# Performance work log

Hardware: AMD Instinct MI355X
Metric: run time of the kernel (lower is better)

## Reference

```python
import jax, jax.numpy as jnp
import numpy as np
from functools import partial

# --- constants from module init / yolov5 NMS conventions ---
CONF_THRES = 0.25
IOU_THRES = 0.45
PATCH_CONF = 0.001
GN = jnp.array([640.0, 640.0, 640.0, 640.0])  # img_size[[1,0,1,0]]
MAX_WH = 4096.0       # per-class NMS offset trick
K_CLEAN = 256         # fixed-size cap for clean detections (max_det=1000 effectively)
K_PATCH = 1024        # fixed-size cap for patch detections (max_det=30000 effectively)
MAXDET_CLEAN = 1000
MAXDET_PATCH = 30000
B, N, NC = 8, 25200, 80


def xywh2xyxy(x):
    xy, wh = x[..., :2], x[..., 2:4]
    return jnp.concatenate([xy - wh * 0.5, xy + wh * 0.5], axis=-1)


def pairwise_iou(a, b):
    # a: [A,4], b: [B,4] -> [A,B] jaccard overlap (same math as IoU.get_iou)
    tl = jnp.maximum(a[:, None, :2], b[None, :, :2])
    br = jnp.minimum(a[:, None, 2:], b[None, :, 2:])
    wh = jnp.clip(br - tl, 0.0)
    inter = wh[..., 0] * wh[..., 1]
    area_a = (a[:, 2] - a[:, 0]) * (a[:, 3] - a[:, 1])
    area_b = (b[:, 2] - b[:, 0]) * (b[:, 3] - b[:, 1])
    return inter / (area_a[:, None] + area_b[None, :] - inter)


def greedy_nms(iou_mat, valid, iou_thres):
    # iou_mat: [K,K] (score-sorted order), valid: [K] bool. Greedy suppression.
    K = valid.shape[0]
    j = jnp.arange(K)

    def body(i, keep):
        suppress = keep[i] & (iou_mat[i] > iou_thres) & (j > i)
        return keep & ~suppress

    return jax.lax.fori_loop(0, K, body, valid)


def _nms_single(pred, conf_thres, K, max_det):
    # pred: [N, 5+nc] raw yolov5 prediction for one image
    boxes = xywh2xyxy(pred[:, :4])
    obj = pred[:, 4]
    cls_scores = pred[:, 5:] * obj[:, None]          # conf = obj * cls
    conf = cls_scores.max(axis=-1)
    cls = jnp.argmax(cls_scores, axis=-1).astype(pred.dtype)
    valid = (obj > conf_thres) & (conf > conf_thres)
    mscore = jnp.where(valid, conf, -1.0)
    _, idx = jax.lax.top_k(mscore, K)                # fixed-size candidate prefilter
    bk, ck, vk = boxes[idx], cls[idx], valid[idx]
    off_boxes = bk + (ck * MAX_WH)[:, None]          # class-offset NMS
    iou = pairwise_iou(off_boxes, off_boxes)
    keep = greedy_nms(jax.lax.stop_gradient(iou), vk, IOU_THRES)
    keep = keep & (jnp.cumsum(keep.astype(jnp.int32)) <= max_det)
    return bk, ck, keep


def _forward(output_clean, output_patch):
    nms_clean = jax.vmap(lambda p: _nms_single(p, CONF_THRES, K_CLEAN, MAXDET_CLEAN))
    nms_patch = jax.vmap(lambda p: _nms_single(p, PATCH_CONF, K_PATCH, MAXDET_PATCH))
    bc, cc, kc = nms_clean(output_clean)   # [B,Kc,4],[B,Kc],[B,Kc]
    bp, cp, kp = nms_patch(output_patch)   # [B,Kp,4],[B,Kp],[B,Kp]
    bc_n = bc / GN
    bp_n = bp / GN

    def per_img(bp_i, cp_i, kp_i, bc_i, cc_i, kc_i):
        iou = pairwise_iou(bp_i, bc_i)                       # [Kp, Kc]
        match = kp_i[:, None] & (cp_i[:, None] == cc_i[None, :])
        tm = jnp.max(jnp.where(match, iou, 0.0), axis=0)     # max IoU per clean det
        return jnp.sum(jnp.where(kc_i, tm, 0.0)), jnp.sum(kc_i.astype(jnp.float32))

    sums, counts = jax.vmap(per_img)(bp_n, cp, kp, bc_n, cc, kc)
    total, cnt = sums.sum(), counts.sum()
    return jnp.where(cnt > 0, 1.0 - total / jnp.maximum(cnt, 1.0), 1.0)


def setup_inputs() -> dict:
    key = jax.random.key(0)
    k1, k2 = jax.random.split(key)

    def make(k):
        kxy, kwh, ko, kc = jax.random.split(k, 4)
        xy = jax.random.uniform(kxy, (B, N, 2)) * 608.0 + 16.0   # centers in-frame
        wh = jax.random.uniform(kwh, (B, N, 2)) * 96.0 + 8.0     # plausible box sizes
        obj = jax.random.uniform(ko, (B, N, 1))
        cls = jax.random.uniform(kc, (B, N, NC))
        return jnp.concatenate([xy, wh, obj, cls], axis=-1)

    return {"output_clean": make(k1), "output_patch": make(k2)}


def reference(output_clean, output_patch):
    return _forward(output_clean, output_patch)
```

## Files before the change

kernel.cpp:

```cpp
#include <hip/hip_runtime.h>

#define N_ANCH 25200
#define NCLS   80
#define ROW    85
#define NIMG   16
#define KMAX   1024
#define NBINS  4096
#define CAND_CAP 4096
#define SC2_RPC 16
#define SC2_CPI 1575
#define SC2_CHUNKS (NIMG * SC2_CPI)
#define SC2_CFLOATS (SC2_RPC * ROW)
#define SC2_BLOCKS 1792
#define PCHUNK 64
#define CCNT_STRIDE 16

typedef unsigned long long u64;
typedef unsigned int u32;

#define OFF_KEYS 0ull
#define OFF_HIST 3225600ull
#define OFF_TBIN 3487744ull
#define OFF_CCNT 3487808ull
#define OFF_SUMS 3488832ull
#define OFF_CNTS 3488864ull
#define OFF_CAND 3488896ull
#define OFF_SEL  4013184ull
#define OFF_BOX  4144256ull
#define OFF_CLS  4406400ull
#define OFF_RINIT 4471936ull
#define OFF_KEEP 4473984ull
#define WS_NEED  4539520ull
#define ZERO_BYTES (262144ull + 64 + 1024 + 32 + 32)

#define DMA16(gsrc, ldst) \
    __builtin_amdgcn_global_load_lds( \
        (const __attribute__((address_space(1))) void*)(gsrc), \
        (__attribute__((address_space(3))) void*)(ldst), 16, 0, 0)

__device__ __forceinline__ int key_bin(u64 key) {
    u32 hi = (u32)(key >> 32);
    if (hi == 0u) return 0;
    float conf = __uint_as_float(hi - 0x40000000u);
    int b = 1 + (int)(conf * 4093.0f);
    return b > 4094 ? 4094 : b;
}

__device__ __forceinline__ u64 readlane64(u64 v, int src) {
    u32 lo = (u32)__builtin_amdgcn_readlane((int)(u32)(v & 0xffffffffull), src);
    u32 hi = (u32)__builtin_amdgcn_readlane((int)(u32)(v >> 32), src);
    return ((u64)hi << 32) | (u64)lo;
}

__device__ __forceinline__ u64 shfl64_xor(u64 v, int m) {
    int lo = __shfl_xor((int)(u32)(v & 0xffffffffull), m, 64);
    int hi = __shfl_xor((int)(u32)(v >> 32), m, 64);
    return ((u64)(u32)hi << 32) | (u64)(u32)lo;
}

__device__ __forceinline__ void sc_issue(const float* __restrict__ clean,
                                         const float* __restrict__ patch,
                                         int c, int lane, float* buf)
{
    const int b = c / SC2_CPI;
    const int ch = c - b * SC2_CPI;
    const float* g = ((b < 8) ? clean + (size_t)b * N_ANCH * ROW
                              : patch + (size_t)(b - 8) * N_ANCH * ROW)
                     + (size_t)ch * SC2_CFLOATS;
    #pragma unroll
    for (int u = 0; u < 5; ++u)
        DMA16(g + u * 256 + lane * 4, buf + u * 256);
    if (lane < 20)
        DMA16(g + 5 * 256 + lane * 4, buf + 5 * 256);
}

__device__ __forceinline__ void sc_compute(int c, int lane,
                                           const float* buf, u64* __restrict__ keys)
{
    const int b = c / SC2_CPI;
    const int ch = c - b * SC2_CPI;
    const int r = lane & 15, h = lane >> 4;
    const float* p = buf + r * ROW;
    const float obj = p[4];
    float best = -1.0f; int bc = 0;
    #pragma unroll
    for (int d = 0; d < 20; ++d) {
        const float s = p[5 + h * 20 + d] * obj;
        if (s > best) { best = s; bc = h * 20 + d; }
    }
    #pragma unroll
    for (int m = 16; m <= 32; m <<= 1) {
        const float o = __shfl_xor(best, m, 64);
        const int  oc = __shfl_xor(bc, m, 64);
        if (o > best || (o == best && oc < bc)) { best = o; bc = oc; }
    }
    if (h == 0) {
        const int n = ch * SC2_RPC + r;
        const float th = (b < 8) ? 0.25f : 0.001f;
        const bool valid = (obj > th) && (best > th);
        const u32 hi = valid ? (__float_as_uint(best) + 0x40000000u) : 0u;
        const u32 nbar = 32767u - (u32)n;
        keys[(size_t)b * N_ANCH + n] =
            ((u64)hi << 32) | ((u64)nbar << 8) | (u64)(u32)bc;
    }
}

__global__ __launch_bounds__(128) void k_score(const float* __restrict__ clean,
                                               const float* __restrict__ patch,
                                               u64* __restrict__ keys)
{
    __shared__ float lds[2][2][SC2_CFLOATS];
    const int wv = threadIdx.x >> 6, lane = threadIdx.x & 63;
    const int wid = blockIdx.x * 2 + wv;
    const int stride = SC2_BLOCKS * 2;
    int cur = 0;
    sc_issue(clean, patch, wid, lane, &lds[wv][0][0]);
    for (int c = wid; c < SC2_CHUNKS; c += stride) {
        const int cn = c + stride;
        if (cn < SC2_CHUNKS) {
            sc_issue(clean, patch, cn, lane, &lds[wv][cur ^ 1][0]);
            asm volatile("s_waitcnt vmcnt(6)" ::: "memory");
        } else {
            asm volatile("s_waitcnt vmcnt(0)" ::: "memory");
        }
        __builtin_amdgcn_sched_barrier(0);
        sc_compute(c, lane, &lds[wv][cur][0], keys);
        cur ^= 1;
    }
}

__global__ __launch_bounds__(256) void k_hist(const u64* __restrict__ keys,
                                              int* __restrict__ hist)
{
    __shared__ int h[NBINS];
    const int b = blockIdx.x;
    for (int i = threadIdx.x; i < NBINS; i += 256) h[i] = 0;
    __syncthreads();
    const int start = blockIdx.y * 1575;
    const u64* kp = keys + (size_t)b * N_ANCH;
    for (int i = start + threadIdx.x; i < start + 1575; i += 256)
        atomicAdd(&h[key_bin(kp[i])], 1);
    __syncthreads();
    for (int i = threadIdx.x; i < NBINS; i += 256)
        if (h[i]) atomicAdd(&hist[b * NBINS + i], h[i]);
}

__global__ __launch_bounds__(1024) void k_thresh(const int* __restrict__ hist,
                                                 int* __restrict__ tbin)
{
    __shared__ int arr[1024];
    const int b = blockIdx.x;
    const int t = threadIdx.x;
    int hh[4];
    hh[0] = hist[b * NBINS + 4 * t + 0];
    hh[1] = hist[b * NBINS + 4 * t + 1];
    hh[2] = hist[b * NBINS + 4 * t + 2];
    hh[3] = hist[b * NBINS + 4 * t + 3];
    const int r = hh[0] + hh[1] + hh[2] + hh[3];
    arr[t] = r;
    __syncthreads();
    for (int off = 1; off < 1024; off <<= 1) {
        int v = (t + off < 1024) ? arr[t + off] : 0;
        __syncthreads();
        arr[t] += v;
        __syncthreads();
    }
    const int K = (b < 8) ? 256 : 1024;
    int cb = arr[t] - r;
    for (int d = 3; d >= 0; --d) {
        int ca = cb + hh[d];
        if (cb < K && ca >= K) tbin[b] = 4 * t + d;
        cb = ca;
    }
}

__global__ __launch_bounds__(256) void k_compact(const u64* __restrict__ keys,
                                                 const int* __restrict__ tbin,
                                                 int* __restrict__ ccnt,
                                                 u64* __restrict__ cand)
{
    const int b = blockIdx.x;
    const int T = tbin[b];
    const u64* kp = keys + (size_t)b * N_ANCH;
    const int start = blockIdx.y * 1575;
    const int lane = threadIdx.x & 63;
    #pragma unroll
    for (int it = 0; it < 7; ++it) {
        const int off = it * 256 + threadIdx.x;
        const bool in = off < 1575;
        const u64 key = in ? kp[start + off] : 0ull;
        const bool cnd = in && (key_bin(key) >= T);
        const u64 bal = __ballot(cnd);
        if (bal) {
            int base = 0;
            if (lane == 0) base = atomicAdd(&ccnt[b * CCNT_STRIDE], __popcll(bal));
            base = __shfl(base, 0, 64);
            if (cnd) {
                const int pos = base + __popcll(bal & ((1ull << lane) - 1ull));
                if (pos < CAND_CAP) cand[(size_t)b * CAND_CAP + pos] = key;
            }
        }
    }
}

__global__ __launch_bounds__(1024) void k_sort(const u64* __restrict__ cand,
                                               const int* __restrict__ ccnt,
                                               u64* __restrict__ sel)
{
    __shared__ u64 sk[CAND_CAP];
    const int b = blockIdx.x;
    const int C = min(ccnt[b * CCNT_STRIDE], CAND_CAP);
    const int t = threadIdx.x;
    u64 e0, e1, e2, e3;
    e0 = (t < C) ? cand[(size_t)b * CAND_CAP + t] : 0ull;
    e1 = (1024 + t < C) ? cand[(size_t)b * CAND_CAP + 1024 + t] : 0ull;
    e2 = (2048 + t < C) ? cand[(size_t)b * CAND_CAP + 2048 + t] : 0ull;
    e3 = (3072 + t < C) ? cand[(size_t)b * CAND_CAP + 3072 + t] : 0ull;

    #define CSWAP_D(a, c) { if ((a) < (c)) { u64 _t = (a); (a) = (c); (c) = _t; } }
    #define CSWAP_A(a, c) { if ((a) > (c)) { u64 _t = (a); (a) = (c); (c) = _t; } }

    for (int k = 2; k <= 4096; k <<= 1) {
        for (int j = k >> 1; j > 0; j >>= 1) {
            if (j >= 1024) {
                if (j == 2048) {
                    CSWAP_D(e0, e2); CSWAP_D(e1, e3);
                } else {
                    if (k == 4096) { CSWAP_D(e0, e1); CSWAP_D(e2, e3); }
                    else           { CSWAP_D(e0, e1); CSWAP_A(e2, e3); }
                }
            } else if (j >= 64) {
                __syncthreads();
                sk[t] = e0; sk[1024 + t] = e1; sk[2048 + t] = e2; sk[3072 + t] = e3;
                __syncthreads();
                const int tp = t ^ j;
                #pragma unroll
                for (int p = 0; p < 4; ++p) {
                    const int i = p * 1024 + t;
                    const u64 cv = (p == 0) ? e0 : (p == 1) ? e1 : (p == 2) ? e2 : e3;
                    const u64 o = sk[p * 1024 + tp];
                    const bool take_max = (((i & k) == 0) == ((t & j) == 0));
                    const u64 mx = cv > o ? cv : o;
                    const u64 mn = cv > o ? o : cv;
                    const u64 nv = take_max ? mx : mn;
                    if (p == 0) e0 = nv; else if (p == 1) e1 = nv;
                    else if (p == 2) e2 = nv; else e3 = nv;
                }
            } else {
                #pragma unroll
                for (int p = 0; p < 4; ++p) {
                    const int i = p * 1024 + t;
                    const u64 cv = (p == 0) ? e0 : (p == 1) ? e1 : (p == 2) ? e2 : e3;
                    const u64 o = shfl64_xor(cv, j);
                    const bool take_max = (((i & k) == 0) == ((t & j) == 0));
                    const u64 mx = cv > o ? cv : o;
                    const u64 mn = cv > o ? o : cv;
                    const u64 nv = take_max ? mx : mn;
                    if (p == 0) e0 = nv; else if (p == 1) e1 = nv;
                    else if (p == 2) e2 = nv; else e3 = nv;
                }
            }
        }
    }
    const int K = (b < 8) ? 256 : 1024;
    if (t < K) sel[b * KMAX + t] = e0;
    #undef CSWAP_D
    #undef CSWAP_A
}

__global__ __launch_bounds__(1024) void k_gather(const float* __restrict__ clean,
                                                 const float* __restrict__ patch,
                                                 const u64* __restrict__ sel,
                                                 float4* __restrict__ boxes,
                                                 int* __restrict__ cls,
                                                 u64* __restrict__ rinit)
{
    const int b = blockIdx.x;
    const int t = threadIdx.x;
    const int K = (b < 8) ? 256 : 1024;
    const u64 key = (t < K) ? sel[b * KMAX + t] : 0ull;
    const u32 hi = (u32)(key >> 32);
    const bool valid = (t < K) && (hi != 0u);
    u64 bal = __ballot(valid);
    if ((t & 63) == 0) rinit[b * 16 + (t >> 6)] = ~bal;
    if (t >= K) return;
    const int n = 32767 - (int)((key >> 8) & 0x7FFFu);
    const int c = (int)(key & 0x7Fu);
    const float* src = ((b < 8) ? (clean + (size_t)b * N_ANCH * ROW)
                                : (patch + (size_t)(b - 8) * N_ANCH * ROW)) + (size_t)n * ROW;
    const float x = src[0], y = src[1], w = src[2], h = src[3];
    boxes[b * KMAX + t] = make_float4(x - w * 0.5f, y - h * 0.5f, x + w * 0.5f, y + h * 0.5f);
    cls[b * KMAX + t] = c;
}

__global__ __launch_bounds__(1024) void k_nms_mask(const float4* __restrict__ boxes,
                                                   const int* __restrict__ cls,
                                                   u64* __restrict__ mask,
                                                   u64* __restrict__ diag)
{
    __shared__ float4 bx[KMAX];
    __shared__ float ar[KMAX];
    const int b = blockIdx.x;
    const int K = (b < 8) ? 256 : 1024;
    const int row0 = blockIdx.y * 64;
    if (row0 >= K) return;
    const int t = threadIdx.x;
    for (int i = t; i < K; i += 1024) {
        float4 v = boxes[b * KMAX + i];
        float off = (float)cls[b * KMAX + i] * 4096.0f;
        v.x += off; v.y += off; v.z += off; v.w += off;
        bx[i] = v;
        ar[i] = (v.z - v.x) * (v.w - v.y);
    }
    __syncthreads();
    const int w   = t >> 6;
    const int row = row0 + (t & 63);
    u64* dst = mask + ((size_t)b * KMAX + row) * 16 + w;
    if (((w << 6) + 63) <= row0 && row0 > 0) { *dst = 0ull; return; }
    const float4 bi = bx[row];
    const float ai = ar[row];
    const int jbase = w << 6;
    u64 m = 0;
    #pragma unroll 8
    for (int k = 0; k < 64; ++k) {
        const int j = jbase + k;
        const float4 bj = bx[j];
        const float ax = fmaxf(bi.x, bj.x), ay = fmaxf(bi.y, bj.y);
        const float bx2 = fminf(bi.z, bj.z), by2 = fminf(bi.w, bj.w);
        const float iw = fmaxf(bx2 - ax, 0.f), ih = fmaxf(by2 - ay, 0.f);
        const float inter = iw * ih;
        const float iou = inter / (ai + ar[j] - inter);
        if (j > row && iou > 0.45f) m |= (1ull << k);
    }
    *dst = m;
    if (w == (row0 >> 6)) diag[(size_t)b * KMAX + row] = m;
}

__global__ __launch_bounds__(1024) void k_nms_scan(const u64* __restrict__ mask,
                                                   const u64* __restrict__ diag,
                                                   const u64* __restrict__ rinit,
                                                   int* __restrict__ keep)
{
    extern __shared__ u64 smem[];
    const int b = blockIdx.x;
    const int K = (b < 8) ? 256 : 1024;
    const int W = K >> 6;
    const int t = threadIdx.x;
    u64* smask = smem;
    u64* sdiag = smem + (size_t)K * 16;
    {
        const float4* s4 = (const float4*)(mask + (size_t)b * KMAX * 16);
        float4* d4 = (float4*)smask;
        const int n4 = (K * 16) >> 1;
        for (int i = t; i < n4; i += 1024) d4[i] = s4[i];
        const float4* s4d = (const float4*)(diag + (size_t)b * KMAX);
        float4* d4d = (float4*)sdiag;
        for (int i = t; i < (K >> 1); i += 1024) d4d[i] = s4d[i];
    }
    __syncthreads();
    if (t >= 64) return;
    const int lane = t;
    const int q = lane >> 4;
    const int wl = lane & 15;
    u64 w_remv = rinit[b * 16 + wl];
    u64 ow = readlane64(w_remv, 0);
    u64 dj = sdiag[lane];
    for (int g = 0; g < W; ++g) {
        u64 nz = __ballot(dj != 0ull);
        u64 o = ow;
        while (nz) {
            const int j = (int)__builtin_ctzll(nz);
            nz &= nz - 1;
            if (!((o >> j) & 1ull)) o |= readlane64(dj, j);
        }
        const u64 kept = ~o;
        if (g + 1 < W) dj = sdiag[(g + 1) * 64 + lane];
        const u64* mrow = smask + (size_t)(g * 64 + q * 16) * 16 + wl;
        const u32 kg = (u32)((kept >> (q * 16)) & 0xFFFFull);
        u64 a0 = 0, a1 = 0;
        #pragma unroll
        for (int i = 0; i < 16; i += 2) {
            const u64 m0 = mrow[(size_t)(i + 0) * 16];
            const u64 m1 = mrow[(size_t)(i + 1) * 16];
            a0 |= ((kg >> i) & 1u) ? m0 : 0ull;
            a1 |= ((kg >> (i + 1)) & 1u) ? m1 : 0ull;
        }
        u64 part = a0 | a1;
        part |= shfl64_xor(part, 16);
        part |= shfl64_xor(part, 32);
        w_remv |= part;
        if (g + 1 < W) ow = readlane64(w_remv, g + 1);
    }
    if (lane < W) {
        #pragma unroll
        for (int k = 0; k < 64; ++k)
            keep[b * KMAX + lane * 64 + k] = (int)(((w_remv >> k) & 1) ^ 1ull);
    }
}

__global__ __launch_bounds__(256) void k_match_partial(const float4* __restrict__ boxes,
                                                       const int* __restrict__ cls,
                                                       const int* __restrict__ keep,
                                                       float* __restrict__ pmax)
{
    __shared__ float4 pb[PCHUNK];
    __shared__ float par[PCHUNK];
    __shared__ int pcls[PCHUNK];
    const int c = blockIdx.x;
    const int p = blockIdx.y;
    const int bp = 8 + c;
    const int t = threadIdx.x;
    if (t < PCHUNK) {
        const int i = p * PCHUNK + t;
        const float4 v = boxes[bp * KMAX + i];
        pb[t] = v;
        par[t] = (v.z - v.x) * (v.w - v.y);
        pcls[t] = keep[bp * KMAX + i] ? cls[bp * KMAX + i] : -1;
    }
    __syncthreads();
    const float4 bc = boxes[c * KMAX + t];
    const int cc = cls[c * KMAX + t];
    const float area_c = (bc.z - bc.x) * (bc.w - bc.y);
    float tm = 0.f;
    #pragma unroll 8
    for (int i = 0; i < PCHUNK; ++i) {
        const float4 bi = pb[i];
        const float ax = fmaxf(bi.x, bc.x), ay = fmaxf(bi.y, bc.y);
        const float bx2 = fminf(bi.z, bc.z), by2 = fminf(bi.w, bc.w);
        const float iw = fmaxf(bx2 - ax, 0.f), ih = fmaxf(by2 - ay, 0.f);
        const float inter = iw * ih;
        const float iou = inter / (par[i] + area_c - inter);
        tm = fmaxf(tm, (pcls[i] == cc) ? iou : 0.f);
    }
    pmax[(c * 16 + p) * 256 + t] = tm;
}

__global__ __launch_bounds__(256) void k_match_reduce(const float* __restrict__ pmax,
                                                      const int* __restrict__ keep,
                                                      float* __restrict__ sums,
                                                      float* __restrict__ cnts)
{
    __shared__ float red[8];
    const int c = blockIdx.x;
    const int t = threadIdx.x;
    float tm = 0.f;
    #pragma unroll
    for (int p = 0; p < 16; ++p)
        tm = fmaxf(tm, pmax[(c * 16 + p) * 256 + t]);
    const int kc = keep[c * KMAX + t];
    float val = kc ? tm : 0.f;
    float cv  = kc ? 1.f : 0.f;
    for (int off = 32; off > 0; off >>= 1) {
        val += __shfl_down(val, off);
        cv  += __shfl_down(cv, off);
    }
    const int wv = t >> 6, lane = t & 63;
    if (lane == 0) { red[wv] = val; red[4 + wv] = cv; }
    __syncthreads();
    if (t == 0) {
        sums[c] = red[0] + red[1] + red[2] + red[3];
        cnts[c] = red[4] + red[5] + red[6] + red[7];
    }
}

__global__ void k_final(const float* __restrict__ sums,
                        const float* __restrict__ cnts,
                        float* __restrict__ out)
{
    if (threadIdx.x == 0 && blockIdx.x == 0) {
        float total = 0.f, cnt = 0.f;
        for (int c = 0; c < 8; ++c) { total += sums[c]; cnt += cnts[c]; }
        out[0] = (cnt > 0.f) ? (1.0f - total / fmaxf(cnt, 1.0f)) : 1.0f;
    }
}

extern "C" void kernel_launch(void* const* d_in, const int* in_sizes, int n_in,
                              void* d_out, int out_size, void* d_ws, size_t ws_size,
                              hipStream_t stream)
{
    if (ws_size < WS_NEED) return;
    const float* clean = (const float*)d_in[0];
    const float* patch = (const float*)d_in[1];
    float* out = (float*)d_out;
    char* ws = (char*)d_ws;

    u64*    keys = (u64*)(ws + OFF_KEYS);
    u64*    mask = (u64*)(ws + OFF_KEYS);
    int*    hist = (int*)(ws + OFF_HIST);
    u64*    diag = (u64*)(ws + OFF_HIST);
    int*    tbin = (int*)(ws + OFF_TBIN);
    int*    ccnt = (int*)(ws + OFF_CCNT);
    float*  sums = (float*)(ws + OFF_SUMS);
    float*  cnts = (float*)(ws + OFF_CNTS);
    u64*    cand = (u64*)(ws + OFF_CAND);
    float*  pmax = (float*)(ws + OFF_CAND);
    u64*    sel  = (u64*)(ws + OFF_SEL);
    float4* boxes = (float4*)(ws + OFF_BOX);
    int*    cls  = (int*)(ws + OFF_CLS);
    u64*    rinit = (u64*)(ws + OFF_RINIT);
    int*    keep = (int*)(ws + OFF_KEEP);

    hipMemsetAsync(ws + OFF_HIST, 0, ZERO_BYTES, stream);

    k_score<<<SC2_BLOCKS, 128, 0, stream>>>(clean, patch, keys);
    k_hist<<<dim3(NIMG, 16), 256, 0, stream>>>(keys, hist);
    k_thresh<<<NIMG, 1024, 0, stream>>>(hist, tbin);
    k_compact<<<dim3(NIMG, 16), 256, 0, stream>>>(keys, tbin, ccnt, cand);
    k_sort<<<NIMG, 1024, 0, stream>>>(cand, ccnt, sel);
    k_gather<<<NIMG, 1024, 0, stream>>>(clean, patch, sel, boxes, cls, rinit);
    k_nms_mask<<<dim3(NIMG, 16), 1024, 0, stream>>>(boxes, cls, mask, diag);
    k_nms_scan<<<NIMG, 1024, KMAX * 16 * 8 + KMAX * 8, stream>>>(mask, diag, rinit, keep);
    k_match_partial<<<dim3(8, 16), 256, 0, stream>>>(boxes, cls, keep, pmax);
    k_match_reduce<<<8, 256, 0, stream>>>(pmax, keep, sums, cnts);
    k_final<<<1, 64, 0, stream>>>(sums, cnts, out);
}
```

Before: 136.1 us.

## Fuse NMS pipeline into four kernels using last-block-done ticket counters

Eleven kernel launches become four. Histogramming and threshold selection move into the scoring kernel, compaction is merged with the bitonic sort, gather is merged with mask build and scan, and the match partial/reduce/final steps are merged, with each tail stage run by the last block to arrive via atomic ticket counters and threadfences. The scoring kernel now assigns a fixed set of blocks to each image, and the histogram is coarsened from 4096 to 1024 bins. This is meant to remove launch overhead and inter-kernel gaps, but serial tails now run in a single block. The coarser bins may also admit more candidates into the sort.

```diff
diff --git a/kernel.cpp b/kernel.cpp
--- a/kernel.cpp
+++ b/kernel.cpp
@@ -5,13 +5,13 @@
 #define ROW    85
 #define NIMG   16
 #define KMAX   1024
-#define NBINS  4096
+#define NBINS  1024
 #define CAND_CAP 4096
 #define SC2_RPC 16
 #define SC2_CPI 1575
-#define SC2_CHUNKS (NIMG * SC2_CPI)
-#define SC2_CFLOATS (SC2_RPC * ROW)
-#define SC2_BLOCKS 1792
+#define SC2_CFLOATS (SC2_RPC*ROW)
+#define SC2_BPI 96
+#define SC2_WPI 192
 #define PCHUNK 64
 #define CCNT_STRIDE 16
 
@@ -20,18 +20,19 @@
 
 #define OFF_KEYS 0ull
 #define OFF_HIST 3225600ull
-#define OFF_TBIN 3487744ull
-#define OFF_CCNT 3487808ull
-#define OFF_SUMS 3488832ull
-#define OFF_CNTS 3488864ull
-#define OFF_CAND 3488896ull
-#define OFF_SEL  4013184ull
-#define OFF_BOX  4144256ull
-#define OFF_CLS  4406400ull
-#define OFF_RINIT 4471936ull
-#define OFF_KEEP 4473984ull
-#define WS_NEED  4539520ull
-#define ZERO_BYTES (262144ull + 64 + 1024 + 32 + 32)
+#define OFF_TBIN 3291136ull
+#define OFF_CCNT 3291200ull
+#define OFF_SUMS 3292224ull
+#define OFF_CNTS 3292256ull
+#define OFF_TICK 3292288ull
+#define OFF_CAND 3292544ull
+#define OFF_SEL  3816832ull
+#define OFF_BOX  3947904ull
+#define OFF_CLS  4210048ull
+#define OFF_RINIT 4275584ull
+#define OFF_KEEP 4277632ull
+#define WS_NEED  4343168ull
+#define ZERO_BYTES 66944ull
 
 #define DMA16(gsrc, ldst) \
     __builtin_amdgcn_global_load_lds( \
@@ -42,8 +43,8 @@
     u32 hi = (u32)(key >> 32);
     if (hi == 0u) return 0;
     float conf = __uint_as_float(hi - 0x40000000u);
-    int b = 1 + (int)(conf * 4093.0f);
-    return b > 4094 ? 4094 : b;
+    int b = 1 + (int)(conf * 1022.0f);
+    return b > 1023 ? 1023 : b;
 }
 
 __device__ __forceinline__ u64 readlane64(u64 v, int src) {
@@ -58,27 +59,20 @@
     return ((u64)(u32)hi << 32) | (u64)(u32)lo;
 }
 
-__device__ __forceinline__ void sc_issue(const float* __restrict__ clean,
-                                         const float* __restrict__ patch,
-                                         int c, int lane, float* buf)
-{
-    const int b = c / SC2_CPI;
-    const int ch = c - b * SC2_CPI;
-    const float* g = ((b < 8) ? clean + (size_t)b * N_ANCH * ROW
-                              : patch + (size_t)(b - 8) * N_ANCH * ROW)
-                     + (size_t)ch * SC2_CFLOATS;
+__device__ __forceinline__ void sc_issue(const float* __restrict__ img, int ch,
+                                         int lane, float* buf)
+{
+    const float* s = img + (size_t)ch * SC2_CFLOATS;
     #pragma unroll
     for (int u = 0; u < 5; ++u)
-        DMA16(g + u * 256 + lane * 4, buf + u * 256);
+        DMA16(s + u * 256 + lane * 4, buf + u * 256);
     if (lane < 20)
-        DMA16(g + 5 * 256 + lane * 4, buf + 5 * 256);
-}
-
-__device__ __forceinline__ void sc_compute(int c, int lane,
-                                           const float* buf, u64* __restrict__ keys)
-{
-    const int b = c / SC2_CPI;
-    const int ch = c - b * SC2_CPI;
+        DMA16(s + 1280 + lane * 4, buf + 1280);
+}
+
+__device__ __forceinline__ void sc_compute(int b, int c, int lane, const float* buf,
+                                           u64* __restrict__ keys, int* bh)
+{
     const int r = lane & 15, h = lane >> 4;
     const float* p = buf + r * ROW;
     const float obj = p[4];
@@ -95,10 +89,13 @@
         if (o > best || (o == best && oc < bc)) { best = o; bc = oc; }
     }
     if (h == 0) {
-        const int n = ch * SC2_RPC + r;
+        const int n = c * SC2_RPC + r;
         const float th = (b < 8) ? 0.25f : 0.001f;
         const bool valid = (obj > th) && (best > th);
         const u32 hi = valid ? (__float_as_uint(best) + 0x40000000u) : 0u;
+        int bin = 0;
+        if (valid) { bin = 1 + (int)(best * 1022.0f); if (bin > 1023) bin = 1023; }
+        atomicAdd(&bh[bin], 1);
         const u32 nbar = 32767u - (u32)n;
         keys[(size_t)b * N_ANCH + n] =
             ((u64)hi << 32) | ((u64)nbar << 8) | (u64)(u32)bc;
@@ -107,88 +104,84 @@
 
 __global__ __launch_bounds__(128) void k_score(const float* __restrict__ clean,
                                                const float* __restrict__ patch,
-                                               u64* __restrict__ keys)
+                                               u64* __restrict__ keys,
+                                               int* __restrict__ hist,
+                                               int* __restrict__ tbin,
+                                               int* __restrict__ tick)
 {
     __shared__ float lds[2][2][SC2_CFLOATS];
-    const int wv = threadIdx.x >> 6, lane = threadIdx.x & 63;
-    const int wid = blockIdx.x * 2 + wv;
-    const int stride = SC2_BLOCKS * 2;
+    __shared__ int bh[NBINS];
+    __shared__ int tks;
+    const int t = threadIdx.x;
+    const int wv = t >> 6, lane = t & 63;
+    const int b = blockIdx.x / SC2_BPI;
+    const int blk = blockIdx.x - b * SC2_BPI;
+    const int wimg = blk * 2 + wv;
+    for (int i = t; i < NBINS; i += 128) bh[i] = 0;
+    __syncthreads();
+    const float* img = (b < 8) ? clean + (size_t)b * N_ANCH * ROW
+                               : patch + (size_t)(b - 8) * N_ANCH * ROW;
     int cur = 0;
-    sc_issue(clean, patch, wid, lane, &lds[wv][0][0]);
-    for (int c = wid; c < SC2_CHUNKS; c += stride) {
-        const int cn = c + stride;
-        if (cn < SC2_CHUNKS) {
-            sc_issue(clean, patch, cn, lane, &lds[wv][cur ^ 1][0]);
+    sc_issue(img, wimg, lane, &lds[wv][0][0]);
+    for (int c = wimg; c < SC2_CPI; c += SC2_WPI) {
+        const int cn = c + SC2_WPI;
+        if (cn < SC2_CPI) {
+            sc_issue(img, cn, lane, &lds[wv][cur ^ 1][0]);
             asm volatile("s_waitcnt vmcnt(6)" ::: "memory");
         } else {
             asm volatile("s_waitcnt vmcnt(0)" ::: "memory");
         }
         __builtin_amdgcn_sched_barrier(0);
-        sc_compute(c, lane, &lds[wv][cur][0], keys);
+        sc_compute(b, c, lane, &lds[wv][cur][0], keys, bh);
         cur ^= 1;
     }
-}
-
-__global__ __launch_bounds__(256) void k_hist(const u64* __restrict__ keys,
-                                              int* __restrict__ hist)
-{
-    __shared__ int h[NBINS];
+    __syncthreads();
+    for (int i = t; i < NBINS; i += 128)
+        if (bh[i]) atomicAdd(&hist[b * NBINS + i], bh[i]);
+    __threadfence();
+    if (t == 0) tks = atomicAdd(&tick[b], 1);
+    __syncthreads();
+    if (tks != SC2_BPI - 1) return;
+    __threadfence();
+    int h8[8]; int s = 0;
+    #pragma unroll
+    for (int d = 0; d < 8; ++d) { h8[d] = hist[b * NBINS + 8 * t + d]; s += h8[d]; }
+    bh[t] = s;
+    __syncthreads();
+    for (int off = 1; off < 128; off <<= 1) {
+        int v = (t + off < 128) ? bh[t + off] : 0;
+        __syncthreads();
+        bh[t] += v;
+        __syncthreads();
+    }
+    const int K = (b < 8) ? 256 : 1024;
+    int cb = bh[t] - s;
+    for (int d = 7; d >= 0; --d) {
+        int ca = cb + h8[d];
+        if (cb < K && ca >= K) tbin[b] = 8 * t + d;
+        cb = ca;
+    }
+}
+
+__global__ __launch_bounds__(1024) void k_csort(const u64* __restrict__ keys,
+                                                const int* __restrict__ tbin,
+                                                int* __restrict__ ccnt,
+                                                u64* __restrict__ cand,
+                                                u64* __restrict__ sel,
+                                                int* __restrict__ tick)
+{
+    __shared__ u64 sk[CAND_CAP];
+    __shared__ int tks;
     const int b = blockIdx.x;
-    for (int i = threadIdx.x; i < NBINS; i += 256) h[i] = 0;
-    __syncthreads();
-    const int start = blockIdx.y * 1575;
-    const u64* kp = keys + (size_t)b * N_ANCH;
-    for (int i = start + threadIdx.x; i < start + 1575; i += 256)
-        atomicAdd(&h[key_bin(kp[i])], 1);
-    __syncthreads();
-    for (int i = threadIdx.x; i < NBINS; i += 256)
-        if (h[i]) atomicAdd(&hist[b * NBINS + i], h[i]);
-}
-
-__global__ __launch_bounds__(1024) void k_thresh(const int* __restrict__ hist,
-                                                 int* __restrict__ tbin)
-{
-    __shared__ int arr[1024];
-    const int b = blockIdx.x;
-    const int t = threadIdx.x;
-    int hh[4];
-    hh[0] = hist[b * NBINS + 4 * t + 0];
-    hh[1] = hist[b * NBINS + 4 * t + 1];
-    hh[2] = hist[b * NBINS + 4 * t + 2];
-    hh[3] = hist[b * NBINS + 4 * t + 3];
-    const int r = hh[0] + hh[1] + hh[2] + hh[3];
-    arr[t] = r;
-    __syncthreads();
-    for (int off = 1; off < 1024; off <<= 1) {
-        int v = (t + off < 1024) ? arr[t + off] : 0;
-        __syncthreads();
-        arr[t] += v;
-        __syncthreads();
-    }
-    const int K = (b < 8) ? 256 : 1024;
-    int cb = arr[t] - r;
-    for (int d = 3; d >= 0; --d) {
-        int ca = cb + hh[d];
-        if (cb < K && ca >= K) tbin[b] = 4 * t + d;
-        cb = ca;
-    }
-}
-
-__global__ __launch_bounds__(256) void k_compact(const u64* __restrict__ keys,
-                                                 const int* __restrict__ tbin,
-                                                 int* __restrict__ ccnt,
-                                                 u64* __restrict__ cand)
-{
-    const int b = blockIdx.x;
+    const int t = threadIdx.x, lane = t & 63;
     const int T = tbin[b];
     const u64* kp = keys + (size_t)b * N_ANCH;
     const int start = blockIdx.y * 1575;
-    const int lane = threadIdx.x & 63;
-    #pragma unroll
-    for (int it = 0; it < 7; ++it) {
-        const int off = it * 256 + threadIdx.x;
-        const bool in = off < 1575;
-        const u64 key = in ? kp[start + off] : 0ull;
+    #pragma unroll
+    for (int it = 0; it < 2; ++it) {
+        const int o = it * 1024 + t;
+        const bool in = o < 1575;
+        const u64 key = in ? kp[start + o] : 0ull;
         const bool cnd = in && (key_bin(key) >= T);
         const u64 bal = __ballot(cnd);
         if (bal) {
@@ -201,31 +194,24 @@
             }
         }
     }
-}
-
-__global__ __launch_bounds__(1024) void k_sort(const u64* __restrict__ cand,
-                                               const int* __restrict__ ccnt,
-                                               u64* __restrict__ sel)
-{
-    __shared__ u64 sk[CAND_CAP];
-    const int b = blockIdx.x;
+    __threadfence();
+    if (t == 0) tks = atomicAdd(&tick[b], 1);
+    __syncthreads();
+    if (tks != 15) return;
+    __threadfence();
     const int C = min(ccnt[b * CCNT_STRIDE], CAND_CAP);
-    const int t = threadIdx.x;
     u64 e0, e1, e2, e3;
     e0 = (t < C) ? cand[(size_t)b * CAND_CAP + t] : 0ull;
     e1 = (1024 + t < C) ? cand[(size_t)b * CAND_CAP + 1024 + t] : 0ull;
     e2 = (2048 + t < C) ? cand[(size_t)b * CAND_CAP + 2048 + t] : 0ull;
     e3 = (3072 + t < C) ? cand[(size_t)b * CAND_CAP + 3072 + t] : 0ull;
-
     #define CSWAP_D(a, c) { if ((a) < (c)) { u64 _t = (a); (a) = (c); (c) = _t; } }
     #define CSWAP_A(a, c) { if ((a) > (c)) { u64 _t = (a); (a) = (c); (c) = _t; } }
-
     for (int k = 2; k <= 4096; k <<= 1) {
         for (int j = k >> 1; j > 0; j >>= 1) {
             if (j >= 1024) {
-                if (j == 2048) {
-                    CSWAP_D(e0, e2); CSWAP_D(e1, e3);
-                } else {
+                if (j == 2048) { CSWAP_D(e0, e2); CSWAP_D(e1, e3); }
+                else {
                     if (k == 4096) { CSWAP_D(e0, e1); CSWAP_D(e2, e3); }
                     else           { CSWAP_D(e0, e1); CSWAP_A(e2, e3); }
                 }
@@ -268,86 +254,80 @@
     #undef CSWAP_A
 }
 
-__global__ __launch_bounds__(1024) void k_gather(const float* __restrict__ clean,
-                                                 const float* __restrict__ patch,
-                                                 const u64* __restrict__ sel,
-                                                 float4* __restrict__ boxes,
-                                                 int* __restrict__ cls,
-                                                 u64* __restrict__ rinit)
-{
-    const int b = blockIdx.x;
+__global__ __launch_bounds__(1024) void k_nms(const float* __restrict__ clean,
+                                              const float* __restrict__ patch,
+                                              const u64* __restrict__ sel,
+                                              float4* __restrict__ boxes,
+                                              int* __restrict__ cls,
+                                              u64* __restrict__ rinit,
+                                              u64* __restrict__ mask,
+                                              u64* __restrict__ diag,
+                                              int* __restrict__ keep,
+                                              int* __restrict__ tick)
+{
+    extern __shared__ u64 dyn[];
+    __shared__ int tkn;
+    const int b = blockIdx.x, y = blockIdx.y;
+    const int K = (b < 8) ? 256 : 1024;
     const int t = threadIdx.x;
-    const int K = (b < 8) ? 256 : 1024;
-    const u64 key = (t < K) ? sel[b * KMAX + t] : 0ull;
-    const u32 hi = (u32)(key >> 32);
-    const bool valid = (t < K) && (hi != 0u);
-    u64 bal = __ballot(valid);
-    if ((t & 63) == 0) rinit[b * 16 + (t >> 6)] = ~bal;
-    if (t >= K) return;
-    const int n = 32767 - (int)((key >> 8) & 0x7FFFu);
-    const int c = (int)(key & 0x7Fu);
-    const float* src = ((b < 8) ? (clean + (size_t)b * N_ANCH * ROW)
-                                : (patch + (size_t)(b - 8) * N_ANCH * ROW)) + (size_t)n * ROW;
-    const float x = src[0], y = src[1], w = src[2], h = src[3];
-    boxes[b * KMAX + t] = make_float4(x - w * 0.5f, y - h * 0.5f, x + w * 0.5f, y + h * 0.5f);
-    cls[b * KMAX + t] = c;
-}
-
-__global__ __launch_bounds__(1024) void k_nms_mask(const float4* __restrict__ boxes,
-                                                   const int* __restrict__ cls,
-                                                   u64* __restrict__ mask,
-                                                   u64* __restrict__ diag)
-{
-    __shared__ float4 bx[KMAX];
-    __shared__ float ar[KMAX];
-    const int b = blockIdx.x;
-    const int K = (b < 8) ? 256 : 1024;
-    const int row0 = blockIdx.y * 64;
-    if (row0 >= K) return;
-    const int t = threadIdx.x;
-    for (int i = t; i < K; i += 1024) {
-        float4 v = boxes[b * KMAX + i];
-        float off = (float)cls[b * KMAX + i] * 4096.0f;
-        v.x += off; v.y += off; v.z += off; v.w += off;
-        bx[i] = v;
-        ar[i] = (v.z - v.x) * (v.w - v.y);
-    }
-    __syncthreads();
-    const int w   = t >> 6;
-    const int row = row0 + (t & 63);
-    u64* dst = mask + ((size_t)b * KMAX + row) * 16 + w;
-    if (((w << 6) + 63) <= row0 && row0 > 0) { *dst = 0ull; return; }
-    const float4 bi = bx[row];
-    const float ai = ar[row];
-    const int jbase = w << 6;
-    u64 m = 0;
-    #pragma unroll 8
-    for (int k = 0; k < 64; ++k) {
-        const int j = jbase + k;
-        const float4 bj = bx[j];
-        const float ax = fmaxf(bi.x, bj.x), ay = fmaxf(bi.y, bj.y);
-        const float bx2 = fminf(bi.z, bj.z), by2 = fminf(bi.w, bj.w);
-        const float iw = fmaxf(bx2 - ax, 0.f), ih = fmaxf(by2 - ay, 0.f);
-        const float inter = iw * ih;
-        const float iou = inter / (ai + ar[j] - inter);
-        if (j > row && iou > 0.45f) m |= (1ull << k);
-    }
-    *dst = m;
-    if (w == (row0 >> 6)) diag[(size_t)b * KMAX + row] = m;
-}
-
-__global__ __launch_bounds__(1024) void k_nms_scan(const u64* __restrict__ mask,
-                                                   const u64* __restrict__ diag,
-                                                   const u64* __restrict__ rinit,
-                                                   int* __restrict__ keep)
-{
-    extern __shared__ u64 smem[];
-    const int b = blockIdx.x;
-    const int K = (b < 8) ? 256 : 1024;
+    float4* bx = (float4*)dyn;
+    float*  ar = (float*)(dyn + 2048);
+    {
+        const u64 key = (t < K) ? sel[b * KMAX + t] : 0ull;
+        const u32 hi = (u32)(key >> 32);
+        const bool valid = (t < K) && (hi != 0u);
+        const u64 bal = __ballot(valid);
+        if (y == 0 && (t & 63) == 0) rinit[b * 16 + (t >> 6)] = ~bal;
+        if (t < K) {
+            const int n = 32767 - (int)((key >> 8) & 0x7FFFu);
+            const int c = (int)(key & 0x7Fu);
+            const float* src = ((b < 8) ? (clean + (size_t)b * N_ANCH * ROW)
+                                        : (patch + (size_t)(b - 8) * N_ANCH * ROW))
+                               + (size_t)n * ROW;
+            const float x = src[0], yy = src[1], w = src[2], h = src[3];
+            const float4 raw = make_float4(x - w * 0.5f, yy - h * 0.5f,
+                                           x + w * 0.5f, yy + h * 0.5f);
+            if (y == 0) { boxes[b * KMAX + t] = raw; cls[b * KMAX + t] = c; }
+            const float off = (float)c * 4096.0f;
+            const float4 ob = make_float4(raw.x + off, raw.y + off, raw.z + off, raw.w + off);
+            bx[t] = ob;
+            ar[t] = (ob.z - ob.x) * (ob.w - ob.y);
+        }
+    }
+    __syncthreads();
+    const int row0 = y * 64;
+    if (row0 < K) {
+        const int w = t >> 6;
+        const int row = row0 + (t & 63);
+        u64 m = 0;
+        const bool skip = (((w << 6) + 63) <= row0) && (row0 > 0);
+        if (!skip) {
+            const float4 bi = bx[row];
+            const float ai = ar[row];
+            const int jbase = w << 6;
+            #pragma unroll 8
+            for (int k2 = 0; k2 < 64; ++k2) {
+                const int j = jbase + k2;
+                const float4 bj = bx[j];
+                const float ax = fmaxf(bi.x, bj.x), ay = fmaxf(bi.y, bj.y);
+                const float bx2 = fminf(bi.z, bj.z), by2 = fminf(bi.w, bj.w);
+                const float iw = fmaxf(bx2 - ax, 0.f), ih = fmaxf(by2 - ay, 0.f);
+                const float inter = iw * ih;
+                const float iou = inter / (ai + ar[j] - inter);
+                if (j > row && iou > 0.45f) m |= (1ull << k2);
+            }
+        }
+        mask[((size_t)b * KMAX + row) * 16 + w] = m;
+        if (w == (row0 >> 6)) diag[(size_t)b * KMAX + row] = m;
+    }
+    __threadfence();
+    if (t == 0) tkn = atomicAdd(&tick[b], 1);
+    __syncthreads();
+    if (tkn != 15) return;
+    __threadfence();
     const int W = K >> 6;
-    const int t = threadIdx.x;
-    u64* smask = smem;
-    u64* sdiag = smem + (size_t)K * 16;
+    u64* smask = dyn;
+    u64* sdiag = dyn + (size_t)K * 16;
     {
         const float4* s4 = (const float4*)(mask + (size_t)b * KMAX * 16);
         float4* d4 = (float4*)smask;
@@ -393,21 +373,27 @@
     }
     if (lane < W) {
         #pragma unroll
-        for (int k = 0; k < 64; ++k)
-            keep[b * KMAX + lane * 64 + k] = (int)(((w_remv >> k) & 1) ^ 1ull);
-    }
-}
-
-__global__ __launch_bounds__(256) void k_match_partial(const float4* __restrict__ boxes,
-                                                       const int* __restrict__ cls,
-                                                       const int* __restrict__ keep,
-                                                       float* __restrict__ pmax)
+        for (int k2 = 0; k2 < 64; ++k2)
+            keep[b * KMAX + lane * 64 + k2] = (int)(((w_remv >> k2) & 1) ^ 1ull);
+    }
+}
+
+__global__ __launch_bounds__(256) void k_match(const float4* __restrict__ boxes,
+                                               const int* __restrict__ cls,
+                                               const int* __restrict__ keep,
+                                               float* __restrict__ pmax,
+                                               float* __restrict__ sums,
+                                               float* __restrict__ cnts,
+                                               int* __restrict__ tick_m,
+                                               int* __restrict__ tick_f,
+                                               float* __restrict__ out)
 {
     __shared__ float4 pb[PCHUNK];
     __shared__ float par[PCHUNK];
     __shared__ int pcls[PCHUNK];
-    const int c = blockIdx.x;
-    const int p = blockIdx.y;
+    __shared__ float red[8];
+    __shared__ int tkm;
+    const int c = blockIdx.x, p = blockIdx.y;
     const int bp = 8 + c;
     const int t = threadIdx.x;
     if (t < PCHUNK) {
@@ -418,35 +404,32 @@
         pcls[t] = keep[bp * KMAX + i] ? cls[bp * KMAX + i] : -1;
     }
     __syncthreads();
-    const float4 bc = boxes[c * KMAX + t];
-    const int cc = cls[c * KMAX + t];
-    const float area_c = (bc.z - bc.x) * (bc.w - bc.y);
+    {
+        const float4 bc = boxes[c * KMAX + t];
+        const int cc = cls[c * KMAX + t];
+        const float area_c = (bc.z - bc.x) * (bc.w - bc.y);
+        float tm = 0.f;
+        #pragma unroll 8
+        for (int i = 0; i < PCHUNK; ++i) {
+            const float4 bi = pb[i];
+            const float ax = fmaxf(bi.x, bc.x), ay = fmaxf(bi.y, bc.y);
+            const float bx2 = fminf(bi.z, bc.z), by2 = fminf(bi.w, bc.w);
+            const float iw = fmaxf(bx2 - ax, 0.f), ih = fmaxf(by2 - ay, 0.f);
+            const float inter = iw * ih;
+            const float iou = inter / (par[i] + area_c - inter);
+            tm = fmaxf(tm, (pcls[i] == cc) ? iou : 0.f);
+        }
+        pmax[(c * 16 + p) * 256 + t] = tm;
+    }
+    __threadfence();
+    if (t == 0) tkm = atomicAdd(&tick_m[c], 1);
+    __syncthreads();
+    if (tkm != 15) return;
+    __threadfence();
     float tm = 0.f;
-    #pragma unroll 8
-    for (int i = 0; i < PCHUNK; ++i) {
-        const float4 bi = pb[i];
-        const float ax = fmaxf(bi.x, bc.x), ay = fmaxf(bi.y, bc.y);
-        const float bx2 = fminf(bi.z, bc.z), by2 = fminf(bi.w, bc.w);
-        const float iw = fmaxf(bx2 - ax, 0.f), ih = fmaxf(by2 - ay, 0.f);
-        const float inter = iw * ih;
-        const float iou = inter / (par[i] + area_c - inter);
-        tm = fmaxf(tm, (pcls[i] == cc) ? iou : 0.f);
-    }
-    pmax[(c * 16 + p) * 256 + t] = tm;
-}
-
-__global__ __launch_bounds__(256) void k_match_reduce(const float* __restrict__ pmax,
-                                                      const int* __restrict__ keep,
-                                                      float* __restrict__ sums,
-                                                      float* __restrict__ cnts)
-{
-    __shared__ float red[8];
-    const int c = blockIdx.x;
-    const int t = threadIdx.x;
-    float tm = 0.f;
-    #pragma unroll
-    for (int p = 0; p < 16; ++p)
-        tm = fmaxf(tm, pmax[(c * 16 + p) * 256 + t]);
+    #pragma unroll
+    for (int p2 = 0; p2 < 16; ++p2)
+        tm = fmaxf(tm, pmax[(c * 16 + p2) * 256 + t]);
     const int kc = keep[c * KMAX + t];
     float val = kc ? tm : 0.f;
     float cv  = kc ? 1.f : 0.f;
@@ -460,17 +443,14 @@
     if (t == 0) {
         sums[c] = red[0] + red[1] + red[2] + red[3];
         cnts[c] = red[4] + red[5] + red[6] + red[7];
-    }
-}
-
-__global__ void k_final(const float* __restrict__ sums,
-                        const float* __restrict__ cnts,
-                        float* __restrict__ out)
-{
-    if (threadIdx.x == 0 && blockIdx.x == 0) {
-        float total = 0.f, cnt = 0.f;
-        for (int c = 0; c < 8; ++c) { total += sums[c]; cnt += cnts[c]; }
-        out[0] = (cnt > 0.f) ? (1.0f - total / fmaxf(cnt, 1.0f)) : 1.0f;
+        __threadfence();
+        const int f = atomicAdd(tick_f, 1);
+        if (f == 7) {
+            __threadfence();
+            float tot = 0.f, cn = 0.f;
+            for (int i = 0; i < 8; ++i) { tot += sums[i]; cn += cnts[i]; }
+            out[0] = (cn > 0.f) ? (1.0f - tot / fmaxf(cn, 1.0f)) : 1.0f;
+        }
     }
 }
 
@@ -487,12 +467,13 @@
     u64*    keys = (u64*)(ws + OFF_KEYS);
     u64*    mask = (u64*)(ws + OFF_KEYS);
     int*    hist = (int*)(ws + OFF_HIST);
-    u64*    diag = (u64*)(ws + OFF_HIST);
     int*    tbin = (int*)(ws + OFF_TBIN);
     int*    ccnt = (int*)(ws + OFF_CCNT);
     float*  sums = (float*)(ws + OFF_SUMS);
     float*  cnts = (float*)(ws + OFF_CNTS);
+    int*    tick = (int*)(ws + OFF_TICK);
     u64*    cand = (u64*)(ws + OFF_CAND);
+    u64*    diag = (u64*)(ws + OFF_CAND);
     float*  pmax = (float*)(ws + OFF_CAND);
     u64*    sel  = (u64*)(ws + OFF_SEL);
     float4* boxes = (float4*)(ws + OFF_BOX);
@@ -502,15 +483,10 @@
 
     hipMemsetAsync(ws + OFF_HIST, 0, ZERO_BYTES, stream);
 
-    k_score<<<SC2_BLOCKS, 128, 0, stream>>>(clean, patch, keys);
-    k_hist<<<dim3(NIMG, 16), 256, 0, stream>>>(keys, hist);
-    k_thresh<<<NIMG, 1024, 0, stream>>>(hist, tbin);
-    k_compact<<<dim3(NIMG, 16), 256, 0, stream>>>(keys, tbin, ccnt, cand);
-    k_sort<<<NIMG, 1024, 0, stream>>>(cand, ccnt, sel);
-    k_gather<<<NIMG, 1024, 0, stream>>>(clean, patch, sel, boxes, cls, rinit);
-    k_nms_mask<<<dim3(NIMG, 16), 1024, 0, stream>>>(boxes, cls, mask, diag);
-    k_nms_scan<<<NIMG, 1024, KMAX * 16 * 8 + KMAX * 8, stream>>>(mask, diag, rinit, keep);
-    k_match_partial<<<dim3(8, 16), 256, 0, stream>>>(boxes, cls, keep, pmax);
-    k_match_reduce<<<8, 256, 0, stream>>>(pmax, keep, sums, cnts);
-    k_final<<<1, 64, 0, stream>>>(sums, cnts, out);
-}
+    k_score<<<NIMG * SC2_BPI, 128, 0, stream>>>(clean, patch, keys, hist, tbin, tick);
+    k_csort<<<dim3(NIMG, 16), 1024, 0, stream>>>(keys, tbin, ccnt, cand, sel, tick + 16);
+    k_nms<<<dim3(NIMG, 16), 1024, KMAX * 16 * 8 + KMAX * 8, stream>>>(
+        clean, patch, sel, boxes, cls, rinit, mask, diag, keep, tick + 32);
+    k_match<<<dim3(8, 16), 256, 0, stream>>>(boxes, cls, keep, pmax, sums, cnts,
+                                             tick + 48, tick + 56, out);
+}
```

Result: slower. 350.4 us (+157.4%).
